# Kernel optimization log

Hardware: AMD Instinct MI355X
Metric: run time of the kernel (lower is better)

The kernel has to match this reference:

```python
import jax, jax.numpy as jnp
import numpy as np

B, NK = 32, 1024
NUM_SAMPLES = 512
IT_MATCHES = 4
IT_RANSAC = 8
NUM_CORR = 5
INLIER_3D_TH = 0.15
INLIER_REF_TH = 0.15
NUM_REF_STEPS = 4
SCORE_TEMP = 10.0
TH_OUTLIERS = 0.35
MAX_LOSS_NULL = 0.5
SOFT_CLIP_M = 0.5
BETA = 5.0 / INLIER_3D_TH


def _gumbel(key, shape):
    u = jax.random.uniform(key, shape, minval=1e-6, maxval=1.0 - 1e-6)
    return -jnp.log(-jnp.log(u))


def _backproject(cor, d, K):
    # cor [B,S,2], d [B,S,2] (channel 0 is depth), K [B,3,3] -> [B,S,3]
    depth = d[..., :1]
    pts = jnp.concatenate([cor, jnp.ones_like(cor[..., :1])], -1)
    Kinv = jnp.linalg.inv(K)
    rays = jnp.einsum('bij,bsj->bsi', Kinv, pts)
    return depth * rays


def _procrustes(X, Y, w):
    # weighted Kabsch: find R,t with Y ~ R X + t. X,Y [B,N,3], w [B,N]
    wn = w / (jnp.sum(w, -1, keepdims=True) + 1e-8)
    muX = jnp.einsum('bn,bni->bi', wn, X)
    muY = jnp.einsum('bn,bni->bi', wn, Y)
    Xc = X - muX[:, None]
    Yc = Y - muY[:, None]
    H = jnp.einsum('bn,bni,bnj->bij', wn, Xc, Yc)  # [B,3,3]
    U, S, Vt = jnp.linalg.svd(H, full_matrices=False)
    V = jnp.swapaxes(Vt, -1, -2)
    Ut = jnp.swapaxes(U, -1, -2)
    d = jnp.linalg.det(V @ Ut)
    Vm = V * jnp.stack([jnp.ones_like(d), jnp.ones_like(d), d], -1)[:, None, :]
    R = Vm @ Ut
    t = muY - jnp.einsum('bij,bj->bi', R, muX)
    return R, t[:, None, :]


def _dist(X, Y, R, t):
    return jnp.linalg.norm(jnp.einsum('bij,bnj->bni', R, X) + t - Y, axis=-1)


def _pose_loss(R, t, Rgt, tgt):
    cosang = jnp.clip((jnp.einsum('bij,bij->b', R, Rgt) - 1.0) / 2.0, -0.999999, 0.999999)
    ang = jnp.arccos(cosang)
    terr = jnp.linalg.norm(t - tgt, axis=-1)[:, 0]
    sc = lambda x: SOFT_CLIP_M * jnp.tanh(x / SOFT_CLIP_M)
    lr = sc(ang)[:, None]
    lt = sc(terr)[:, None]
    return 0.5 * (lr + lt), lr, lt


def _rodrigues(axis, ang):
    x, y, z = axis[:, 0], axis[:, 1], axis[:, 2]
    zero = jnp.zeros_like(x)
    Kx = jnp.stack([zero, -z, y, z, zero, -x, -y, x, zero], -1).reshape(-1, 3, 3)
    I = jnp.eye(3, dtype=axis.dtype)[None]
    return I + jnp.sin(ang)[:, None, None] * Kx + (1.0 - jnp.cos(ang))[:, None, None] * (Kx @ Kx)


def setup_inputs():
    ks = jax.random.split(jax.random.key(0), 10)
    matches = jax.random.uniform(ks[0], (B, NK, NK), jnp.float32, 1e-4, 1.0)
    kps0 = jax.random.uniform(ks[1], (B, 2, NK), jnp.float32, 0.0, 640.0)
    kps1 = jax.random.uniform(ks[2], (B, 2, NK), jnp.float32, 0.0, 640.0)
    depth0 = jax.random.uniform(ks[3], (B, 2, NK), jnp.float32, 0.1, 10.0)
    depth1 = jax.random.uniform(ks[4], (B, 2, NK), jnp.float32, 0.1, 10.0)
    Kc = jnp.tile(jnp.array([[600.0, 0.0, 320.0], [0.0, 600.0, 240.0], [0.0, 0.0, 1.0]], jnp.float32)[None], (B, 1, 1))
    axis = jax.random.normal(ks[5], (B, 3))
    axis = axis / (jnp.linalg.norm(axis, axis=-1, keepdims=True) + 1e-8)
    ang = jax.random.uniform(ks[6], (B,), minval=0.0, maxval=0.5)
    R = _rodrigues(axis, ang)
    tvec = 0.3 * jax.random.normal(ks[7], (B, 3))
    T = jnp.zeros((B, 4, 4), jnp.float32).at[:, :3, :3].set(R).at[:, :3, 3].set(tvec).at[:, 3, 3].set(1.0)
    return dict(matches=matches, kps0=kps0, depth0=depth0, kps1=kps1, depth1=depth1,
                K0=Kc, K1=Kc, Kori_color0=Kc, T_0to1=T)


def _forward(matches, kps0, depth0, kps1, depth1, K0, K1, T_0to1):
    Rgt = T_0to1[:, :3, :3]
    tgt = T_0to1[:, :3, 3][:, None, :]
    matches_row = matches.reshape(B, NK * NK)
    logm = jnp.log(matches_row + 1e-12)
    bidx = jnp.arange(B)[:, None]
    kps0t = jnp.swapaxes(kps0, 1, 2)  # [B,NK,2]
    kps1t = jnp.swapaxes(kps1, 1, 2)
    d0t = jnp.swapaxes(depth0, 1, 2)
    d1t = jnp.swapaxes(depth1, 1, 2)
    key = jax.random.key(42)
    total = jnp.zeros((B, 1), jnp.float32)
    for _i in range(IT_MATCHES):
        key, km = jax.random.split(key)
        # multinomial-without-replacement via Gumbel top-k over the full match matrix
        _, sidx = jax.lax.top_k(logm + _gumbel(km, logm.shape), NUM_SAMPLES)  # [B,S]
        i0 = sidx // NK
        i1 = sidx % NK
        cor0 = kps0t[bidx, i0]
        cor1 = kps1t[bidx, i1]
        dd0 = d0t[bidx, i0]
        dd1 = d1t[bidx, i1]
        w = matches_row[bidx, sidx]  # sampling weights for RANSAC minimal sets
        X = _backproject(cor0, dd0, K0)
        Y = _backproject(cor1, dd1, K1)
        logw = jnp.log(w + 1e-12)
        scores, lvals = [], []
        for _kk in range(IT_RANSAC):
            key, kr = jax.random.split(key)
            _, ridx = jax.lax.top_k(logw + _gumbel(kr, logw.shape), NUM_CORR)  # [B,C]
            Xk = X[bidx, ridx]
            Yk = Y[bidx, ridx]
            R_pre, t_pre = _procrustes(Xk, Yk, jnp.ones((B, NUM_CORR), X.dtype))  # use_weights=False
            score_k = jnp.sum(jax.nn.sigmoid(BETA * (INLIER_3D_TH - _dist(X, Y, R_pre, t_pre))), -1, keepdims=True)
            # inlier refinement (no_grad in original)
            Xd = jax.lax.stop_gradient(X)
            Yd = jax.lax.stop_gradient(Y)
            Rd = jax.lax.stop_gradient(R_pre)
            td = jax.lax.stop_gradient(t_pre)
            inl_ref = jnp.zeros((B, NUM_SAMPLES), X.dtype).at[bidx, ridx].set(1.0)
            inl_pre = jnp.zeros((B,), X.dtype)
            for _r in range(NUM_REF_STEPS):
                inl = (_dist(Xd, Yd, Rd, td) < INLIER_REF_TH).astype(X.dtype)
                cnt = inl.sum(-1)
                do = (cnt >= NUM_CORR) & (cnt > inl_pre)
                inl_pre = cnt
                inl_ref = jnp.where(do[:, None], inl, inl_ref)
                Rn, tn = _procrustes(Xd, Yd, inl_ref)
                Rd = jnp.where(do[:, None, None], Rn, Rd)
                td = jnp.where(do[:, None, None], tn, td)
            R, t = _procrustes(X, Y, inl_ref)  # differentiable final fit
            lv, _lr, _lt = _pose_loss(R, t, Rgt, tgt)
            scores.append(score_k)
            lvals.append(lv)
        scores_r = jnp.concatenate(scores, -1)  # [B,IT_RANSAC]
        lvals_r = jnp.concatenate(lvals, -1)
        null_score = TH_OUTLIERS * NUM_SAMPLES * jnp.ones((B, 1), jnp.float32)
        null_loss = MAX_LOSS_NULL * jnp.ones((B, 1), jnp.float32)
        scores_n = jnp.concatenate([scores_r, null_score], -1)
        lvals_n = jnp.concatenate([lvals_r, null_loss], -1)
        sm = jax.nn.softmax(scores_n / SCORE_TEMP, -1)
        total = total + jnp.sum(lvals_n * sm, -1, keepdims=True)
    return total / IT_MATCHES


def reference(matches, kps0, depth0, kps1, depth1, K0, K1, Kori_color0, T_0to1):
    return _forward(matches, kps0, depth0, kps1, depth1, K0, K1, T_0to1)
```

## Files before the change

### kernel.cpp

```cpp
#include <hip/hip_runtime.h>
#include <stdint.h>

typedef unsigned long long u64;
typedef uint32_t u32;

#define NB 32
#define NKP 1024
#define ROWN (NKP*NKP)
#define NSAMP 512
#define ITM 4
#define ITR 8
#define NBIN 2048
#define KBASE 0xC0000000u
#define CHUNKS 64
#define SLOTS 256
#define WQ 352

struct Keys { u32 km[ITM][2]; u32 kr[ITM][ITR][2]; };

__host__ __device__ static inline u32 rotl32(u32 x, int d) { return __builtin_rotateleft32(x, (unsigned)d); }

__host__ __device__ static inline void tf2x32(u32 k0, u32 k1, u32 x0, u32 x1, u32& o0, u32& o1)
{
    u32 ks2 = k0 ^ k1 ^ 0x1BD11BDAu;
    x0 += k0; x1 += k1;
#define TFR(r) { x0 += x1; x1 = rotl32(x1, r); x1 ^= x0; }
    TFR(13) TFR(15) TFR(26) TFR(6)
    x0 += k1; x1 += ks2 + 1u;
    TFR(17) TFR(29) TFR(16) TFR(24)
    x0 += ks2; x1 += k0 + 2u;
    TFR(13) TFR(15) TFR(26) TFR(6)
    x0 += k0; x1 += k1 + 3u;
    TFR(17) TFR(29) TFR(16) TFR(24)
    x0 += k1; x1 += ks2 + 4u;
    TFR(13) TFR(15) TFR(26) TFR(6)
    x0 += ks2; x1 += k0 + 5u;
#undef TFR
    o0 = x0; o1 = x1;
}

__device__ static inline void tf4(const Keys& K, u32 flat, u32 bits[ITM])
{
    u32 x0[ITM], x1[ITM];
    #pragma unroll
    for (int i = 0; i < ITM; ++i) {
        x0[i] = K.km[i][0];
        x1[i] = flat + K.km[i][1];
    }
#define R4(rot) { _Pragma("unroll") \
    for (int i = 0; i < ITM; ++i) { x0[i] += x1[i]; x1[i] = rotl32(x1[i], rot); x1[i] ^= x0[i]; } }
#define INJ(a_expr, b_expr) { _Pragma("unroll") \
    for (int i = 0; i < ITM; ++i) { u32 k0 = K.km[i][0], k1 = K.km[i][1]; \
        u32 ks2 = k0 ^ k1 ^ 0x1BD11BDAu; (void)k0; (void)k1; (void)ks2; \
        x0[i] += (a_expr); x1[i] += (b_expr); } }
    R4(13) R4(15) R4(26) R4(6)
    INJ(k1,      ks2 + 1u)
    R4(17) R4(29) R4(16) R4(24)
    INJ(ks2,     k0 + 2u)
    R4(13) R4(15) R4(26) R4(6)
    INJ(k0,      k1 + 3u)
    R4(17) R4(29) R4(16) R4(24)
    INJ(k1,      ks2 + 4u)
    R4(13) R4(15) R4(26) R4(6)
    INJ(ks2,     k0 + 5u)
#undef R4
#undef INJ
    #pragma unroll
    for (int i = 0; i < ITM; ++i) bits[i] = x0[i] ^ x1[i];
}

#define G_MINV 1e-6f
#define G_MAXV ((float)(1.0 - 1e-6))
#define G_SPAN (G_MAXV - G_MINV)

__device__ static inline float u_from_bits(u32 bits) {
    float f = __uint_as_float((bits >> 9) | 0x3f800000u) - 1.0f;
    float u = __fadd_rn(__fmul_rn(f, G_SPAN), G_MINV);
    return fmaxf(G_MINV, u);
}

#define EARLY_TH9 (8220000u << 9)

__device__ static inline u32 fkey(float v) {
    u32 u = __float_as_uint(v);
    return (u & 0x80000000u) ? ~u : (u | 0x80000000u);
}

__device__ static inline float wred(float v) {
    #pragma unroll
    for (int o = 1; o < 64; o <<= 1) v += __shfl_xor(v, o, 64);
    return v;
}

__device__ static inline u64 shfl_xor_u64(u64 v, int mask) {
    u32 lo = (u32)v, hi = (u32)(v >> 32);
    lo = __shfl_xor(lo, mask, 64);
    hi = __shfl_xor(hi, mask, 64);
    return ((u64)hi << 32) | (u64)lo;
}

__device__ static void kabsch(const float Hf[9], float Rf[9])
{
    double H00=Hf[0],H01=Hf[1],H02=Hf[2];
    double H10=Hf[3],H11=Hf[4],H12=Hf[5];
    double H20=Hf[6],H21=Hf[7],H22=Hf[8];
    double A00 = H00*H00 + H10*H10 + H20*H20;
    double A01 = H00*H01 + H10*H11 + H20*H21;
    double A02 = H00*H02 + H10*H12 + H20*H22;
    double A11 = H01*H01 + H11*H11 + H21*H21;
    double A12 = H01*H02 + H11*H12 + H21*H22;
    double A22 = H02*H02 + H12*H12 + H22*H22;
    double V00=1,V10=0,V20=0;
    double V01=0,V11=1,V21=0;
    double V02=0,V12=0,V22=1;
#define JROT(App,Aqq,Apq,Apr,Aqr, Vp0,Vp1,Vp2, Vq0,Vq1,Vq2) \
    if (fabs(Apq) > 0.0) { \
        double th = (Aqq - App) / (2.0 * Apq); \
        double tt = copysign(1.0, th) / (fabs(th) + sqrt(1.0 + th*th)); \
        double cc = 1.0 / sqrt(1.0 + tt*tt); \
        double ss = tt * cc; \
        double npp = App - tt*Apq, nqq = Aqq + tt*Apq; \
        double npr = cc*Apr - ss*Aqr, nqr = ss*Apr + cc*Aqr; \
        App = npp; Aqq = nqq; Apq = 0.0; Apr = npr; Aqr = nqr; \
        double tv; \
        tv = cc*Vp0 - ss*Vq0; Vq0 = ss*Vp0 + cc*Vq0; Vp0 = tv; \
        tv = cc*Vp1 - ss*Vq1; Vq1 = ss*Vp1 + cc*Vq1; Vp1 = tv; \
        tv = cc*Vp2 - ss*Vq2; Vq2 = ss*Vp2 + cc*Vq2; Vp2 = tv; \
    }
    for (int sw = 0; sw < 5; ++sw) {
        JROT(A00,A11,A01, A02,A12, V00,V10,V20, V01,V11,V21);
        JROT(A00,A22,A02, A01,A12, V00,V10,V20, V02,V12,V22);
        JROT(A11,A22,A12, A01,A02, V01,V11,V21, V02,V12,V22);
    }
#undef JROT
    double l0=A00, l1=A11, l2=A22;
    double e0[3]={V00,V10,V20}, e1[3]={V01,V11,V21}, e2[3]={V02,V12,V22};
    if (l0 < l1) { double t=l0;l0=l1;l1=t; for(int c=0;c<3;++c){double s=e0[c];e0[c]=e1[c];e1[c]=s;} }
    if (l0 < l2) { double t=l0;l0=l2;l2=t; for(int c=0;c<3;++c){double s=e0[c];e0[c]=e2[c];e2[c]=s;} }
    if (l1 < l2) { double t=l1;l1=l2;l2=t; for(int c=0;c<3;++c){double s=e1[c];e1[c]=e2[c];e2[c]=s;} }
    double u0[3], u1[3], u2[3];
#define HMUL(e,u) { u[0]=H00*e[0]+H01*e[1]+H02*e[2]; u[1]=H10*e[0]+H11*e[1]+H12*e[2]; u[2]=H20*e[0]+H21*e[1]+H22*e[2]; }
    HMUL(e0,u0) HMUL(e1,u1) HMUL(e2,u2)
#undef HMUL
    double s0 = sqrt(u0[0]*u0[0]+u0[1]*u0[1]+u0[2]*u0[2]);
    double s1 = sqrt(u1[0]*u1[0]+u1[1]*u1[1]+u1[2]*u1[2]);
    double s2 = sqrt(u2[0]*u2[0]+u2[1]*u2[1]+u2[2]*u2[2]);
    double eps = 1e-12 + 1e-6 * s0;
    if (s0 > 0.0) { u0[0]/=s0; u0[1]/=s0; u0[2]/=s0; } else { u0[0]=1.0; u0[1]=0.0; u0[2]=0.0; }
    if (s1 > eps) { u1[0]/=s1; u1[1]/=s1; u1[2]/=s1; }
    else {
        double ax0 = (fabs(u0[0]) < 0.9) ? 1.0 : 0.0;
        double ax1 = 1.0 - ax0;
        double dd = ax0*u0[0] + ax1*u0[1];
        double w0 = ax0 - dd*u0[0], w1 = ax1 - dd*u0[1], w2 = -dd*u0[2];
        double nn = sqrt(w0*w0+w1*w1+w2*w2);
        u1[0]=w0/nn; u1[1]=w1/nn; u1[2]=w2/nn;
    }
    if (s2 > eps) { u2[0]/=s2; u2[1]/=s2; u2[2]/=s2; }
    else {
        u2[0] = u0[1]*u1[2] - u0[2]*u1[1];
        u2[1] = u0[2]*u1[0] - u0[0]*u1[2];
        u2[2] = u0[0]*u1[1] - u0[1]*u1[0];
    }
    double M[3][3];
    #pragma unroll
    for (int i2=0;i2<3;++i2)
      #pragma unroll
      for (int j2=0;j2<3;++j2)
        M[i2][j2] = e0[i2]*u0[j2] + e1[i2]*u1[j2] + e2[i2]*u2[j2];
    double det = M[0][0]*(M[1][1]*M[2][2]-M[1][2]*M[2][1])
               - M[0][1]*(M[1][0]*M[2][2]-M[1][2]*M[2][0])
               + M[0][2]*(M[1][0]*M[2][1]-M[1][1]*M[2][0]);
    #pragma unroll
    for (int i2=0;i2<3;++i2)
      #pragma unroll
      for (int j2=0;j2<3;++j2)
        Rf[i2*3+j2] = (float)(e0[i2]*u0[j2] + e1[i2]*u1[j2] + det*(e2[i2]*u2[j2]));
}

__device__ static inline float dist1(const float R[9], const float t[3], const float x[3], const float y[3])
{
    float a = R[0]*x[0]+R[1]*x[1]+R[2]*x[2]+t[0]-y[0];
    float b = R[3]*x[0]+R[4]*x[1]+R[5]*x[2]+t[1]-y[1];
    float c = R[6]*x[0]+R[7]*x[1]+R[8]*x[2]+t[2]-y[2];
    return sqrtf(a*a+b*b+c*c);
}

__device__ static void proc512(const float (&X)[8][3], const float (&Y)[8][3], const float (&w)[8],
                               float R[9], float t[3])
{
    float sw = 0.f;
    #pragma unroll
    for (int q=0;q<8;++q) sw += w[q];
    float S = wred(sw) + 1e-8f;
    float wn[8];
    #pragma unroll
    for (int q=0;q<8;++q) wn[q] = w[q] / S;
    float mx[3], my[3];
    #pragma unroll
    for (int c=0;c<3;++c) {
        float ax=0.f, ay=0.f;
        #pragma unroll
        for (int q=0;q<8;++q) { ax += wn[q]*X[q][c]; ay += wn[q]*Y[q][c]; }
        mx[c] = wred(ax); my[c] = wred(ay);
    }
    float Hf[9];
    #pragma unroll
    for (int ci=0;ci<3;++ci)
      #pragma unroll
      for (int cj=0;cj<3;++cj) {
        float h=0.f;
        #pragma unroll
        for (int q=0;q<8;++q) h += wn[q]*(X[q][ci]-mx[ci])*(Y[q][cj]-my[cj]);
        Hf[ci*3+cj] = wred(h);
      }
    kabsch(Hf, R);
    #pragma unroll
    for (int c=0;c<3;++c) t[c] = my[c] - (R[c*3+0]*mx[0] + R[c*3+1]*mx[1] + R[c*3+2]*mx[2]);
}

__device__ static void inv3(const float* __restrict__ Kin, float* __restrict__ out)
{
    float a[3][6];
    for (int r=0;r<3;++r) for (int c=0;c<3;++c) { a[r][c]=Kin[r*3+c]; a[r][c+3] = (r==c)?1.f:0.f; }
    for (int col=0; col<3; ++col) {
        int piv = col;
        for (int r=col+1;r<3;++r) if (fabsf(a[r][col]) > fabsf(a[piv][col])) piv = r;
        if (piv != col) for (int c=0;c<6;++c) { float tt=a[col][c]; a[col][c]=a[piv][c]; a[piv][c]=tt; }
        float pv = a[col][col];
        for (int c=0;c<6;++c) a[col][c] /= pv;
        for (int r=0;r<3;++r) if (r != col) {
            float f = a[r][col];
            if (f != 0.f) for (int c=0;c<6;++c) a[r][c] -= f * a[col][c];
        }
    }
    for (int r=0;r<3;++r) for (int c=0;c<3;++c) out[r*3+c] = a[r][c+3];
}

static const size_t OFF_CNTS = 0;
static const size_t OFF_SC   = OFF_CNTS + (size_t)ITM*NB*CHUNKS*4;
static const size_t OFF_LV   = OFF_SC   + (size_t)ITM*NB*ITR*4;
static const size_t OFF_SAMP = OFF_LV   + (size_t)ITM*NB*ITR*4;
static const size_t OFF_CAND = OFF_SAMP + (size_t)ITM*NB*NSAMP*8*4;

__global__ __launch_bounds__(256) void kA(const float* __restrict__ mat, Keys keys,
                                          u64* __restrict__ candC, u32* __restrict__ cnts)
{
    __shared__ u64 lists[ITM][SLOTS];
    __shared__ u32 lcnt[ITM];
    __shared__ u64 q[4][WQ];
    __shared__ u32 wcnt[4];
    int tid = threadIdx.x;
    int lane = tid & 63;
    int wid = tid >> 6;
    u64 lmask_lt = (1ull << lane) - 1ull;
    if (tid < ITM) lcnt[tid] = 0;
    __syncthreads();
    int b = blockIdx.y;
    int chunk = blockIdx.x;
    const float* rowb = mat + (size_t)b * ROWN;
    u32 jbase = (u32)chunk * 16384u + (u32)tid;
    for (int seg = 0; seg < 2; ++seg) {
        u32 cnt = 0;
        for (int lp = 0; lp < 32; ++lp) {
            u32 j = jbase + (u32)((seg*32 + lp) << 8);
            u32 flat = ((u32)b << 20) | j;
            u32 bits[ITM];
            tf4(keys, flat, bits);
            #pragma unroll
            for (int i = 0; i < ITM; ++i) {
                bool hit = (bits[i] >= EARLY_TH9);
                u64 mask = __ballot(hit);
                if (hit) {
                    u32 pos = cnt + (u32)__popcll(mask & lmask_lt);
                    if (pos < (u32)WQ)
                        q[wid][pos] = ((u64)bits[i] << 32) | ((u64)(u32)i << 20) | (u64)j;
                }
                cnt += (u32)__popcll(mask);
            }
        }
        __syncthreads();
        if (lane == 0) wcnt[wid] = (cnt > (u32)WQ) ? (u32)WQ : cnt;
        __syncthreads();
        for (int w = 0; w < 4; ++w) {
            u32 qn = wcnt[w];
            for (u32 t = tid; t < qn; t += 256) {
                u64 e  = q[w][t];
                u32 bits = (u32)(e >> 32);
                u32 i2 = ((u32)e >> 20) & 3u;
                u32 jj = (u32)e & 0xFFFFFu;
                float m  = rowb[jj];
                float u  = u_from_bits(bits);
                float g  = -logf(-logf(u));
                float v  = logf(m + 1e-12f) + g;
                if (v > 4.0f) {
                    u32 p = atomicAdd(&lcnt[i2], 1u);
                    if (p < (u32)SLOTS)
                        lists[i2][p] = ((u64)fkey(v) << 32) | (u64)(u32)(~jj);
                }
            }
        }
        __syncthreads();
    }
    #pragma unroll
    for (int i = 0; i < ITM; ++i) {
        u32 n = lcnt[i]; if (n > (u32)SLOTS) n = SLOTS;
        for (u32 s = tid; s < n; s += 256)
            candC[(((size_t)(i*NB + b))*CHUNKS + chunk)*SLOTS + s] = lists[i][s];
    }
    if (tid < ITM) cnts[((size_t)(tid*NB + b))*CHUNKS + chunk] = min(lcnt[tid], (u32)SLOTS);
}

__global__ __launch_bounds__(256) void kD(const float* __restrict__ mat,
        const float* __restrict__ kps0, const float* __restrict__ dep0,
        const float* __restrict__ kps1, const float* __restrict__ dep1,
        const float* __restrict__ K0, const float* __restrict__ K1,
        const u64* __restrict__ candC, const u32* __restrict__ cnts,
        float* __restrict__ samp)
{
    int ib = blockIdx.x;
    int b = ib % NB;
    int tid = threadIdx.x;
    __shared__ u32 hist[NBIN];
    __shared__ u64 buf[2048];
    __shared__ u32 ccnt[CHUNKS];
    __shared__ u32 gs[64];
    __shared__ u32 nkeep, cutkey_s;
    __shared__ float Ki[2][9];
    for (int idx = tid; idx < NBIN; idx += 256) hist[idx] = 0;
    for (int idx = tid; idx < 2048; idx += 256) buf[idx] = 0ull;
    if (tid < CHUNKS) ccnt[tid] = cnts[(size_t)ib*CHUNKS + tid];
    if (tid == 0) nkeep = 0;
    __syncthreads();
    const u64* cd = candC + (size_t)ib * CHUNKS * SLOTS;
    for (int t = tid; t < CHUNKS*SLOTS; t += 256) {
        int c = t >> 8, s = t & (SLOTS-1);
        if ((u32)s < ccnt[c]) {
            u32 key = (u32)(cd[t] >> 32);
            u32 bin = (key - KBASE) >> 14;
            if (bin > (u32)(NBIN-1)) bin = NBIN-1;
            atomicAdd(&hist[bin], 1u);
        }
    }
    __syncthreads();
    if (tid < 64) {
        u32 ssum = 0;
        int top = NBIN-1 - tid*32;
        for (int k = 0; k < 32; ++k) ssum += hist[top - k];
        gs[tid] = ssum;
    }
    __syncthreads();
    if (tid == 0) {
        u32 cum = 0; int cutbin = -1;
        for (int g = 0; g < 64; ++g) {
            if (cum + gs[g] >= (u32)NSAMP) {
                int t2 = NBIN-1 - g*32;
                for (int k = 0; k < 32; ++k) {
                    u32 c = hist[t2 - k];
                    if (cum + c >= (u32)NSAMP) { cutbin = t2 - k; break; }
                    cum += c;
                }
                break;
            }
            cum += gs[g];
        }
        cutkey_s = (cutbin >= 0) ? (KBASE + ((u32)cutbin << 14)) : 0u;
    }
    __syncthreads();
    u32 cutkey = cutkey_s;
    for (int t = tid; t < CHUNKS*SLOTS; t += 256) {
        int c = t >> 8, s = t & (SLOTS-1);
        if ((u32)s < ccnt[c]) {
            u64 cv = cd[t];
            if ((u32)(cv >> 32) >= cutkey) {
                u32 p = atomicAdd(&nkeep, 1u);
                if (p < 2048u) buf[p] = cv;
            }
        }
    }
    __syncthreads();
    for (int k = 2; k <= 2048; k <<= 1) {
        for (int j = k >> 1; j > 0; j >>= 1) {
            for (int i2 = tid; i2 < 2048; i2 += 256) {
                int ixj = i2 ^ j;
                if (ixj > i2) {
                    bool up = ((i2 & k) == 0);
                    u64 a = buf[i2], c2 = buf[ixj];
                    bool dosw = up ? (a > c2) : (a < c2);
                    if (dosw) { buf[i2] = c2; buf[ixj] = a; }
                }
            }
            __syncthreads();
        }
    }
    if (tid == 0) { inv3(K0 + (size_t)b*9, Ki[0]); inv3(K1 + (size_t)b*9, Ki[1]); }
    __syncthreads();
    for (int r = tid; r < NSAMP; r += 256) {
        u64 c = buf[2047 - r];
        u32 j = (~(u32)(c & 0xFFFFFFFFull)) & (u32)(ROWN - 1);
        int i0 = (int)(j >> 10);
        int i1 = (int)(j & 1023u);
        float uu0 = kps0[(size_t)b*2*NKP + i0];
        float vv0 = kps0[(size_t)b*2*NKP + NKP + i0];
        float dd0 = dep0[(size_t)b*2*NKP + i0];
        float uu1 = kps1[(size_t)b*2*NKP + i1];
        float vv1 = kps1[(size_t)b*2*NKP + NKP + i1];
        float dd1 = dep1[(size_t)b*2*NKP + i1];
        float r0 = Ki[0][0]*uu0 + Ki[0][1]*vv0 + Ki[0][2];
        float r1 = Ki[0][3]*uu0 + Ki[0][4]*vv0 + Ki[0][5];
        float r2 = Ki[0][6]*uu0 + Ki[0][7]*vv0 + Ki[0][8];
        float q0 = Ki[1][0]*uu1 + Ki[1][1]*vv1 + Ki[1][2];
        float q1 = Ki[1][3]*uu1 + Ki[1][4]*vv1 + Ki[1][5];
        float q2 = Ki[1][6]*uu1 + Ki[1][7]*vv1 + Ki[1][8];
        float w = mat[(size_t)b*ROWN + j];
        float* sp = samp + ((size_t)ib*NSAMP + r)*8;
        sp[0] = dd0*r0; sp[1] = dd0*r1; sp[2] = dd0*r2;
        sp[3] = dd1*q0; sp[4] = dd1*q1; sp[5] = dd1*q2;
        sp[6] = logf(w + 1e-12f);
        sp[7] = 0.f;
    }
}

__global__ __launch_bounds__(64) void kE(const float* __restrict__ samp, const float* __restrict__ Tmat,
                                         Keys keys, float* __restrict__ scoreArr, float* __restrict__ lvArr)
{
    int blk = blockIdx.x;
    int kk = blk & 7;
    int ib = blk >> 3;
    int i = ib / NB;
    int b = ib % NB;
    int lane = threadIdx.x;
    const float* s = samp + (size_t)ib * NSAMP * 8;
    float X[8][3], Y[8][3], lw[8];
    #pragma unroll
    for (int q = 0; q < 8; ++q) {
        const float4* p = reinterpret_cast<const float4*>(s + (size_t)(q*64 + lane)*8);
        float4 a0 = p[0], a1 = p[1];
        X[q][0]=a0.x; X[q][1]=a0.y; X[q][2]=a0.z;
        Y[q][0]=a0.w; Y[q][1]=a1.x; Y[q][2]=a1.y;
        lw[q]=a1.z;
    }
    u64 comp[8];
    #pragma unroll
    for (int q = 0; q < 8; ++q) {
        u32 j = (u32)(q*64 + lane);
        u32 o0,o1; tf2x32(keys.kr[i][kk][0], keys.kr[i][kk][1], 0u, (u32)(b*NSAMP) + j, o0,o1);
        float u = u_from_bits(o0^o1);
        float g = -logf(-logf(u));
        float v = lw[q] + g;
        comp[q] = ((u64)fkey(v) << 32) | (u64)(u32)(~j);
    }
    int ridx[5];
    #pragma unroll
    for (int r = 0; r < 5; ++r) {
        u64 m = comp[0];
        #pragma unroll
        for (int q=1;q<8;++q) if (comp[q] > m) m = comp[q];
        #pragma unroll
        for (int o=1;o<64;o<<=1) { u64 x = shfl_xor_u64(m,o); if (x > m) m = x; }
        ridx[r] = (int)((~(u32)(m & 0xFFFFFFFFull)) & (u32)(NSAMP-1));
        #pragma unroll
        for (int q=0;q<8;++q) if (comp[q] == m) comp[q] = 0ull;
    }
    float Xk[5][3], Yk[5][3];
    #pragma unroll
    for (int r=0;r<5;++r) {
        const float* p = s + (size_t)ridx[r]*8;
        Xk[r][0]=p[0]; Xk[r][1]=p[1]; Xk[r][2]=p[2];
        Yk[r][0]=p[3]; Yk[r][1]=p[4]; Yk[r][2]=p[5];
    }
    float S5 = 5.0f + 1e-8f;
    float wn5 = 1.0f / S5;
    float mx[3]={0,0,0}, my[3]={0,0,0};
    #pragma unroll
    for (int r=0;r<5;++r) {
        #pragma unroll
        for (int c=0;c<3;++c) { mx[c] += wn5*Xk[r][c]; my[c] += wn5*Yk[r][c]; }
    }
    float Hf[9] = {0,0,0,0,0,0,0,0,0};
    #pragma unroll
    for (int r=0;r<5;++r)
      #pragma unroll
      for (int ci=0;ci<3;++ci)
        #pragma unroll
        for (int cj=0;cj<3;++cj)
          Hf[ci*3+cj] += wn5*(Xk[r][ci]-mx[ci])*(Yk[r][cj]-my[cj]);
    float Rpre[9], tpre[3];
    kabsch(Hf, Rpre);
    #pragma unroll
    for (int c=0;c<3;++c) tpre[c] = my[c] - (Rpre[c*3+0]*mx[0] + Rpre[c*3+1]*mx[1] + Rpre[c*3+2]*mx[2]);
    const float BETAF = (float)(5.0/0.15);
    float partial = 0.f;
    #pragma unroll
    for (int q=0;q<8;++q) {
        float d = dist1(Rpre, tpre, X[q], Y[q]);
        float z = BETAF * (0.15f - d);
        partial += 1.0f / (1.0f + expf(-z));
    }
    float score = wred(partial);
    float inlref[8];
    #pragma unroll
    for (int q=0;q<8;++q) {
        int j = q*64 + lane;
        inlref[q] = (j==ridx[0] || j==ridx[1] || j==ridx[2] || j==ridx[3] || j==ridx[4]) ? 1.0f : 0.0f;
    }
    float Rd[9], td[3];
    #pragma unroll
    for (int c2=0;c2<9;++c2) Rd[c2]=Rpre[c2];
    td[0]=tpre[0]; td[1]=tpre[1]; td[2]=tpre[2];
    float inl_pre = 0.f;
    for (int step=0; step<4; ++step) {
        float inl[8]; float csum = 0.f;
        #pragma unroll
        for (int q=0;q<8;++q) {
            float d = dist1(Rd, td, X[q], Y[q]);
            inl[q] = (d < 0.15f) ? 1.0f : 0.0f;
            csum += inl[q];
        }
        float cnt = wred(csum);
        bool doit = (cnt >= 5.0f) && (cnt > inl_pre);
        inl_pre = cnt;
        if (doit) {
            #pragma unroll
            for (int q=0;q<8;++q) inlref[q] = inl[q];
            proc512(X, Y, inlref, Rd, td);
        }
    }
    float Rfin[9], tfin[3];
    proc512(X, Y, inlref, Rfin, tfin);
    const float* Tb = Tmat + (size_t)b*16;
    float tr = 0.f;
    #pragma unroll
    for (int ci=0;ci<3;++ci)
      #pragma unroll
      for (int cj=0;cj<3;++cj)
        tr += Rfin[ci*3+cj] * Tb[ci*4+cj];
    float cosang = (tr - 1.0f) * 0.5f;
    cosang = fminf(fmaxf(cosang, -0.999999f), 0.999999f);
    float ang = acosf(cosang);
    float d0 = tfin[0]-Tb[3], d1 = tfin[1]-Tb[7], d2 = tfin[2]-Tb[11];
    float terr = sqrtf(d0*d0 + d1*d1 + d2*d2);
    float lr = 0.5f * tanhf(ang / 0.5f);
    float lt = 0.5f * tanhf(terr / 0.5f);
    float lv = 0.5f * (lr + lt);
    if (lane == 0) { scoreArr[blk] = score; lvArr[blk] = lv; }
}

__global__ void kF(const float* __restrict__ scoreArr, const float* __restrict__ lvArr, float* __restrict__ out)
{
    int b = threadIdx.x;
    if (b >= NB) return;
    const float NULLSC = (float)(0.35 * 512.0);
    float total = 0.f;
    for (int i = 0; i < ITM; ++i) {
        float x[9], lvv[9], ee[9];
        for (int k = 0; k < 8; ++k) {
            x[k] = scoreArr[(i*NB + b)*ITR + k] / 10.0f;
            lvv[k] = lvArr[(i*NB + b)*ITR + k];
        }
        x[8] = NULLSC / 10.0f;
        lvv[8] = 0.5f;
        float m = x[0];
        for (int k = 1; k < 9; ++k) m = fmaxf(m, x[k]);
        float Ssum = 0.f;
        for (int k = 0; k < 9; ++k) { ee[k] = expf(x[k] - m); Ssum += ee[k]; }
        float acc = 0.f;
        for (int k = 0; k < 9; ++k) acc += lvv[k] * (ee[k] / Ssum);
        total += acc;
    }
    out[b] = total / 4.0f;
}

extern "C" void kernel_launch(void* const* d_in, const int* in_sizes, int n_in,
                              void* d_out, int out_size, void* d_ws, size_t ws_size,
                              hipStream_t stream)
{
    (void)in_sizes; (void)n_in; (void)out_size; (void)ws_size;
    const float* mat  = (const float*)d_in[0];
    const float* kps0 = (const float*)d_in[1];
    const float* dep0 = (const float*)d_in[2];
    const float* kps1 = (const float*)d_in[3];
    const float* dep1 = (const float*)d_in[4];
    const float* K0   = (const float*)d_in[5];
    const float* K1   = (const float*)d_in[6];
    const float* Tm   = (const float*)d_in[8];
    float* out = (float*)d_out;

    Keys keys;
    {
        u32 k0 = 0u, k1 = 42u;
        for (int i = 0; i < ITM; ++i) {
            u32 a0,a1,b0,b1;
            tf2x32(k0,k1, 0u,0u, a0,a1);
            tf2x32(k0,k1, 0u,1u, b0,b1);
            k0=a0; k1=a1; keys.km[i][0]=b0; keys.km[i][1]=b1;
            for (int kk = 0; kk < ITR; ++kk) {
                tf2x32(k0,k1, 0u,0u, a0,a1);
                tf2x32(k0,k1, 0u,1u, b0,b1);
                k0=a0; k1=a1; keys.kr[i][kk][0]=b0; keys.kr[i][kk][1]=b1;
            }
        }
    }
    char* ws = (char*)d_ws;
    u32* cnts       = (u32*)(ws + OFF_CNTS);
    float* scoreArr = (float*)(ws + OFF_SC);
    float* lvArr    = (float*)(ws + OFF_LV);
    float* samp     = (float*)(ws + OFF_SAMP);
    u64* candC      = (u64*)(ws + OFF_CAND);

    kA<<<dim3(CHUNKS, NB), 256, 0, stream>>>(mat, keys, candC, cnts);
    kD<<<ITM*NB, 256, 0, stream>>>(mat, kps0, dep0, kps1, dep1, K0, K1, candC, cnts, samp);
    kE<<<ITM*NB*ITR, 64, 0, stream>>>(samp, Tm, keys, scoreArr, lvArr);
    kF<<<1, 64, 0, stream>>>(scoreArr, lvArr, out);
}
```

Baseline: 394.5 us.

## Fuse sample selection and RANSAC kernels, drain queues per-wave without block barriers

Merges the top-K sample selection kernel and the per-hypothesis RANSAC kernel into one 512-thread block per (iteration, batch). Samples stay in LDS, and each of the 8 waves runs one hypothesis, which removes the global sample buffer round-trip and one launch. The bitonic sort buffer shrinks from 2048 to 1024 entries. In the candidate kernel, each wave drains its own queue with four batched gathers instead of going through block-wide barriers. The smaller sort buffer drops candidates when more than 1024 pass the cutoff. The fused kernel runs only 128 blocks with heavy LDS use, so parallelism is limited.

```diff
diff --git a/kernel.cpp b/kernel.cpp
--- a/kernel.cpp
+++ b/kernel.cpp
@@ -243,13 +243,26 @@
 static const size_t OFF_SAMP = OFF_LV   + (size_t)ITM*NB*ITR*4;
 static const size_t OFF_CAND = OFF_SAMP + (size_t)ITM*NB*NSAMP*8*4;
 
+__device__ static inline void drain1(u64 e, float m, u64 (*lists)[SLOTS], u32* lcnt)
+{
+    u32 bits = (u32)(e >> 32);
+    u32 i2 = ((u32)e >> 20) & 3u;
+    u32 jj = (u32)e & 0xFFFFFu;
+    float u = u_from_bits(bits);
+    float g = -logf(-logf(u));
+    float v = logf(m + 1e-12f) + g;
+    if (v > 4.0f) {
+        u32 p = atomicAdd(&lcnt[i2], 1u);
+        if (p < (u32)SLOTS) lists[i2][p] = ((u64)fkey(v) << 32) | (u64)(u32)(~jj);
+    }
+}
+
 __global__ __launch_bounds__(256) void kA(const float* __restrict__ mat, Keys keys,
                                           u64* __restrict__ candC, u32* __restrict__ cnts)
 {
     __shared__ u64 lists[ITM][SLOTS];
     __shared__ u32 lcnt[ITM];
     __shared__ u64 q[4][WQ];
-    __shared__ u32 wcnt[4];
     int tid = threadIdx.x;
     int lane = tid & 63;
     int wid = tid >> 6;
@@ -262,6 +275,7 @@
     u32 jbase = (u32)chunk * 16384u + (u32)tid;
     for (int seg = 0; seg < 2; ++seg) {
         u32 cnt = 0;
+        #pragma unroll 1
         for (int lp = 0; lp < 32; ++lp) {
             u32 j = jbase + (u32)((seg*32 + lp) << 8);
             u32 flat = ((u32)b << 20) | j;
@@ -279,29 +293,23 @@
                 cnt += (u32)__popcll(mask);
             }
         }
-        __syncthreads();
-        if (lane == 0) wcnt[wid] = (cnt > (u32)WQ) ? (u32)WQ : cnt;
-        __syncthreads();
-        for (int w = 0; w < 4; ++w) {
-            u32 qn = wcnt[w];
-            for (u32 t = tid; t < qn; t += 256) {
-                u64 e  = q[w][t];
-                u32 bits = (u32)(e >> 32);
-                u32 i2 = ((u32)e >> 20) & 3u;
-                u32 jj = (u32)e & 0xFFFFFu;
-                float m  = rowb[jj];
-                float u  = u_from_bits(bits);
-                float g  = -logf(-logf(u));
-                float v  = logf(m + 1e-12f) + g;
-                if (v > 4.0f) {
-                    u32 p = atomicAdd(&lcnt[i2], 1u);
-                    if (p < (u32)SLOTS)
-                        lists[i2][p] = ((u64)fkey(v) << 32) | (u64)(u32)(~jj);
-                }
-            }
-        }
-        __syncthreads();
-    }
+        u32 qn = (cnt > (u32)WQ) ? (u32)WQ : cnt;
+        for (u32 t0 = (u32)lane; t0 < qn; t0 += 256) {
+            u32 t1 = t0 + 64, t2 = t0 + 128, t3 = t0 + 192;
+            u64 e0 = q[wid][t0];
+            float m0 = rowb[(u32)e0 & 0xFFFFFu];
+            u64 e1 = 0, e2 = 0, e3 = 0;
+            float m1 = 0.f, m2 = 0.f, m3 = 0.f;
+            if (t1 < qn) { e1 = q[wid][t1]; m1 = rowb[(u32)e1 & 0xFFFFFu]; }
+            if (t2 < qn) { e2 = q[wid][t2]; m2 = rowb[(u32)e2 & 0xFFFFFu]; }
+            if (t3 < qn) { e3 = q[wid][t3]; m3 = rowb[(u32)e3 & 0xFFFFFu]; }
+            drain1(e0, m0, lists, lcnt);
+            if (t1 < qn) drain1(e1, m1, lists, lcnt);
+            if (t2 < qn) drain1(e2, m2, lists, lcnt);
+            if (t3 < qn) drain1(e3, m3, lists, lcnt);
+        }
+    }
+    __syncthreads();
     #pragma unroll
     for (int i = 0; i < ITM; ++i) {
         u32 n = lcnt[i]; if (n > (u32)SLOTS) n = SLOTS;
@@ -311,29 +319,34 @@
     if (tid < ITM) cnts[((size_t)(tid*NB + b))*CHUNKS + chunk] = min(lcnt[tid], (u32)SLOTS);
 }
 
-__global__ __launch_bounds__(256) void kD(const float* __restrict__ mat,
+__global__ __launch_bounds__(512) void kDE(const float* __restrict__ mat,
         const float* __restrict__ kps0, const float* __restrict__ dep0,
         const float* __restrict__ kps1, const float* __restrict__ dep1,
         const float* __restrict__ K0, const float* __restrict__ K1,
+        const float* __restrict__ Tmat, Keys keys,
         const u64* __restrict__ candC, const u32* __restrict__ cnts,
-        float* __restrict__ samp)
+        float* __restrict__ scoreArr, float* __restrict__ lvArr)
 {
     int ib = blockIdx.x;
     int b = ib % NB;
+    int i = ib / NB;
     int tid = threadIdx.x;
+    int lane = tid & 63;
+    int wid = tid >> 6;
     __shared__ u32 hist[NBIN];
-    __shared__ u64 buf[2048];
+    __shared__ u64 buf[1024];
+    __shared__ float sampL[NSAMP][9];
     __shared__ u32 ccnt[CHUNKS];
     __shared__ u32 gs[64];
     __shared__ u32 nkeep, cutkey_s;
     __shared__ float Ki[2][9];
-    for (int idx = tid; idx < NBIN; idx += 256) hist[idx] = 0;
-    for (int idx = tid; idx < 2048; idx += 256) buf[idx] = 0ull;
+    for (int idx = tid; idx < NBIN; idx += 512) hist[idx] = 0;
+    for (int idx = tid; idx < 1024; idx += 512) buf[idx] = 0ull;
     if (tid < CHUNKS) ccnt[tid] = cnts[(size_t)ib*CHUNKS + tid];
     if (tid == 0) nkeep = 0;
     __syncthreads();
     const u64* cd = candC + (size_t)ib * CHUNKS * SLOTS;
-    for (int t = tid; t < CHUNKS*SLOTS; t += 256) {
+    for (int t = tid; t < CHUNKS*SLOTS; t += 512) {
         int c = t >> 8, s = t & (SLOTS-1);
         if ((u32)s < ccnt[c]) {
             u32 key = (u32)(cd[t] >> 32);
@@ -368,20 +381,20 @@
     }
     __syncthreads();
     u32 cutkey = cutkey_s;
-    for (int t = tid; t < CHUNKS*SLOTS; t += 256) {
+    for (int t = tid; t < CHUNKS*SLOTS; t += 512) {
         int c = t >> 8, s = t & (SLOTS-1);
         if ((u32)s < ccnt[c]) {
             u64 cv = cd[t];
             if ((u32)(cv >> 32) >= cutkey) {
                 u32 p = atomicAdd(&nkeep, 1u);
-                if (p < 2048u) buf[p] = cv;
+                if (p < 1024u) buf[p] = cv;
             }
         }
     }
     __syncthreads();
-    for (int k = 2; k <= 2048; k <<= 1) {
+    for (int k = 2; k <= 1024; k <<= 1) {
         for (int j = k >> 1; j > 0; j >>= 1) {
-            for (int i2 = tid; i2 < 2048; i2 += 256) {
+            for (int i2 = tid; i2 < 1024; i2 += 512) {
                 int ixj = i2 ^ j;
                 if (ixj > i2) {
                     bool up = ((i2 & k) == 0);
@@ -395,77 +408,67 @@
     }
     if (tid == 0) { inv3(K0 + (size_t)b*9, Ki[0]); inv3(K1 + (size_t)b*9, Ki[1]); }
     __syncthreads();
-    for (int r = tid; r < NSAMP; r += 256) {
-        u64 c = buf[2047 - r];
-        u32 j = (~(u32)(c & 0xFFFFFFFFull)) & (u32)(ROWN - 1);
-        int i0 = (int)(j >> 10);
-        int i1 = (int)(j & 1023u);
-        float uu0 = kps0[(size_t)b*2*NKP + i0];
-        float vv0 = kps0[(size_t)b*2*NKP + NKP + i0];
-        float dd0 = dep0[(size_t)b*2*NKP + i0];
-        float uu1 = kps1[(size_t)b*2*NKP + i1];
-        float vv1 = kps1[(size_t)b*2*NKP + NKP + i1];
-        float dd1 = dep1[(size_t)b*2*NKP + i1];
-        float r0 = Ki[0][0]*uu0 + Ki[0][1]*vv0 + Ki[0][2];
-        float r1 = Ki[0][3]*uu0 + Ki[0][4]*vv0 + Ki[0][5];
-        float r2 = Ki[0][6]*uu0 + Ki[0][7]*vv0 + Ki[0][8];
-        float q0 = Ki[1][0]*uu1 + Ki[1][1]*vv1 + Ki[1][2];
-        float q1 = Ki[1][3]*uu1 + Ki[1][4]*vv1 + Ki[1][5];
-        float q2 = Ki[1][6]*uu1 + Ki[1][7]*vv1 + Ki[1][8];
-        float w = mat[(size_t)b*ROWN + j];
-        float* sp = samp + ((size_t)ib*NSAMP + r)*8;
-        sp[0] = dd0*r0; sp[1] = dd0*r1; sp[2] = dd0*r2;
-        sp[3] = dd1*q0; sp[4] = dd1*q1; sp[5] = dd1*q2;
-        sp[6] = logf(w + 1e-12f);
-        sp[7] = 0.f;
-    }
-}
-
-__global__ __launch_bounds__(64) void kE(const float* __restrict__ samp, const float* __restrict__ Tmat,
-                                         Keys keys, float* __restrict__ scoreArr, float* __restrict__ lvArr)
-{
-    int blk = blockIdx.x;
-    int kk = blk & 7;
-    int ib = blk >> 3;
-    int i = ib / NB;
-    int b = ib % NB;
-    int lane = threadIdx.x;
-    const float* s = samp + (size_t)ib * NSAMP * 8;
+    {
+        int r = tid;
+        if (r < NSAMP) {
+            u64 c = buf[1023 - r];
+            u32 j = (~(u32)(c & 0xFFFFFFFFull)) & (u32)(ROWN - 1);
+            int i0 = (int)(j >> 10);
+            int i1 = (int)(j & 1023u);
+            float uu0 = kps0[(size_t)b*2*NKP + i0];
+            float vv0 = kps0[(size_t)b*2*NKP + NKP + i0];
+            float dd0 = dep0[(size_t)b*2*NKP + i0];
+            float uu1 = kps1[(size_t)b*2*NKP + i1];
+            float vv1 = kps1[(size_t)b*2*NKP + NKP + i1];
+            float dd1 = dep1[(size_t)b*2*NKP + i1];
+            float r0 = Ki[0][0]*uu0 + Ki[0][1]*vv0 + Ki[0][2];
+            float r1 = Ki[0][3]*uu0 + Ki[0][4]*vv0 + Ki[0][5];
+            float r2 = Ki[0][6]*uu0 + Ki[0][7]*vv0 + Ki[0][8];
+            float q0 = Ki[1][0]*uu1 + Ki[1][1]*vv1 + Ki[1][2];
+            float q1 = Ki[1][3]*uu1 + Ki[1][4]*vv1 + Ki[1][5];
+            float q2 = Ki[1][6]*uu1 + Ki[1][7]*vv1 + Ki[1][8];
+            float w = mat[(size_t)b*ROWN + j];
+            sampL[r][0] = dd0*r0; sampL[r][1] = dd0*r1; sampL[r][2] = dd0*r2;
+            sampL[r][3] = dd1*q0; sampL[r][4] = dd1*q1; sampL[r][5] = dd1*q2;
+            sampL[r][6] = logf(w + 1e-12f);
+        }
+    }
+    __syncthreads();
+    int kk = wid;
     float X[8][3], Y[8][3], lw[8];
     #pragma unroll
-    for (int q = 0; q < 8; ++q) {
-        const float4* p = reinterpret_cast<const float4*>(s + (size_t)(q*64 + lane)*8);
-        float4 a0 = p[0], a1 = p[1];
-        X[q][0]=a0.x; X[q][1]=a0.y; X[q][2]=a0.z;
-        Y[q][0]=a0.w; Y[q][1]=a1.x; Y[q][2]=a1.y;
-        lw[q]=a1.z;
+    for (int q2 = 0; q2 < 8; ++q2) {
+        const float* sp = &sampL[q2*64 + lane][0];
+        X[q2][0]=sp[0]; X[q2][1]=sp[1]; X[q2][2]=sp[2];
+        Y[q2][0]=sp[3]; Y[q2][1]=sp[4]; Y[q2][2]=sp[5];
+        lw[q2]=sp[6];
     }
     u64 comp[8];
     #pragma unroll
-    for (int q = 0; q < 8; ++q) {
-        u32 j = (u32)(q*64 + lane);
+    for (int q2 = 0; q2 < 8; ++q2) {
+        u32 j = (u32)(q2*64 + lane);
         u32 o0,o1; tf2x32(keys.kr[i][kk][0], keys.kr[i][kk][1], 0u, (u32)(b*NSAMP) + j, o0,o1);
         float u = u_from_bits(o0^o1);
         float g = -logf(-logf(u));
-        float v = lw[q] + g;
-        comp[q] = ((u64)fkey(v) << 32) | (u64)(u32)(~j);
+        float v = lw[q2] + g;
+        comp[q2] = ((u64)fkey(v) << 32) | (u64)(u32)(~j);
     }
     int ridx[5];
     #pragma unroll
     for (int r = 0; r < 5; ++r) {
         u64 m = comp[0];
         #pragma unroll
-        for (int q=1;q<8;++q) if (comp[q] > m) m = comp[q];
+        for (int q2=1;q2<8;++q2) if (comp[q2] > m) m = comp[q2];
         #pragma unroll
         for (int o=1;o<64;o<<=1) { u64 x = shfl_xor_u64(m,o); if (x > m) m = x; }
         ridx[r] = (int)((~(u32)(m & 0xFFFFFFFFull)) & (u32)(NSAMP-1));
         #pragma unroll
-        for (int q=0;q<8;++q) if (comp[q] == m) comp[q] = 0ull;
+        for (int q2=0;q2<8;++q2) if (comp[q2] == m) comp[q2] = 0ull;
     }
     float Xk[5][3], Yk[5][3];
     #pragma unroll
     for (int r=0;r<5;++r) {
-        const float* p = s + (size_t)ridx[r]*8;
+        const float* p = &sampL[ridx[r]][0];
         Xk[r][0]=p[0]; Xk[r][1]=p[1]; Xk[r][2]=p[2];
         Yk[r][0]=p[3]; Yk[r][1]=p[4]; Yk[r][2]=p[5];
     }
@@ -492,17 +495,17 @@
     const float BETAF = (float)(5.0/0.15);
     float partial = 0.f;
     #pragma unroll
-    for (int q=0;q<8;++q) {
-        float d = dist1(Rpre, tpre, X[q], Y[q]);
+    for (int q2=0;q2<8;++q2) {
+        float d = dist1(Rpre, tpre, X[q2], Y[q2]);
         float z = BETAF * (0.15f - d);
         partial += 1.0f / (1.0f + expf(-z));
     }
     float score = wred(partial);
     float inlref[8];
     #pragma unroll
-    for (int q=0;q<8;++q) {
-        int j = q*64 + lane;
-        inlref[q] = (j==ridx[0] || j==ridx[1] || j==ridx[2] || j==ridx[3] || j==ridx[4]) ? 1.0f : 0.0f;
+    for (int q2=0;q2<8;++q2) {
+        int j = q2*64 + lane;
+        inlref[q2] = (j==ridx[0] || j==ridx[1] || j==ridx[2] || j==ridx[3] || j==ridx[4]) ? 1.0f : 0.0f;
     }
     float Rd[9], td[3];
     #pragma unroll
@@ -512,17 +515,17 @@
     for (int step=0; step<4; ++step) {
         float inl[8]; float csum = 0.f;
         #pragma unroll
-        for (int q=0;q<8;++q) {
-            float d = dist1(Rd, td, X[q], Y[q]);
-            inl[q] = (d < 0.15f) ? 1.0f : 0.0f;
-            csum += inl[q];
+        for (int q2=0;q2<8;++q2) {
+            float d = dist1(Rd, td, X[q2], Y[q2]);
+            inl[q2] = (d < 0.15f) ? 1.0f : 0.0f;
+            csum += inl[q2];
         }
         float cnt = wred(csum);
         bool doit = (cnt >= 5.0f) && (cnt > inl_pre);
         inl_pre = cnt;
         if (doit) {
             #pragma unroll
-            for (int q=0;q<8;++q) inlref[q] = inl[q];
+            for (int q2=0;q2<8;++q2) inlref[q2] = inl[q2];
             proc512(X, Y, inlref, Rd, td);
         }
     }
@@ -543,7 +546,7 @@
     float lr = 0.5f * tanhf(ang / 0.5f);
     float lt = 0.5f * tanhf(terr / 0.5f);
     float lv = 0.5f * (lr + lt);
-    if (lane == 0) { scoreArr[blk] = score; lvArr[blk] = lv; }
+    if (lane == 0) { scoreArr[ib*ITR + kk] = score; lvArr[ib*ITR + kk] = lv; }
 }
 
 __global__ void kF(const float* __restrict__ scoreArr, const float* __restrict__ lvArr, float* __restrict__ out)
@@ -605,11 +608,10 @@
     u32* cnts       = (u32*)(ws + OFF_CNTS);
     float* scoreArr = (float*)(ws + OFF_SC);
     float* lvArr    = (float*)(ws + OFF_LV);
-    float* samp     = (float*)(ws + OFF_SAMP);
     u64* candC      = (u64*)(ws + OFF_CAND);
 
     kA<<<dim3(CHUNKS, NB), 256, 0, stream>>>(mat, keys, candC, cnts);
-    kD<<<ITM*NB, 256, 0, stream>>>(mat, kps0, dep0, kps1, dep1, K0, K1, candC, cnts, samp);
-    kE<<<ITM*NB*ITR, 64, 0, stream>>>(samp, Tm, keys, scoreArr, lvArr);
+    kDE<<<ITM*NB, 512, 0, stream>>>(mat, kps0, dep0, kps1, dep1, K0, K1, Tm, keys,
+                                    candC, cnts, scoreArr, lvArr);
     kF<<<1, 64, 0, stream>>>(scoreArr, lvArr, out);
 }
```

Measured after the change: 337.2 us. 14.5% less time.
